# Optimization experiments

Hardware: AMD Instinct MI355X
Metric: run time of the kernel (lower is better)

Reference implementation:

```python
import jax, jax.numpy as jnp
import numpy as np

N, E, M, G = 100000, 1600000, 20000, 512
IN, ED, OUT, H, C = 64, 16, 64, 4, 8


def segment_softmax(alpha, seg, num):
    # alpha: [Etot, H]; softmax over edges sharing the same destination segment
    amax = jax.ops.segment_max(alpha, seg, num_segments=num)
    amax = jnp.where(jnp.isneginf(amax), 0.0, amax)
    ex = jnp.exp(alpha - amax[seg])
    den = jax.ops.segment_sum(ex, seg, num_segments=num)
    return ex / (den[seg] + 1e-16)


def gat_conv(x, src, dst, ea, W, We, a_s, a_d, a_e, b, concat):
    # PyG GATConv: shared lin for src/dst, edge-conditioned attention, self loops pre-added
    n = x.shape[0]
    h, c = a_s.shape
    hx = (x @ W).reshape(n, h, c)            # [N,H,C]
    ee = (ea @ We).reshape(-1, h, c)          # [Etot,H,C]
    alpha = jax.nn.leaky_relu((hx * a_s).sum(-1)[src] + (hx * a_d).sum(-1)[dst] + (ee * a_e).sum(-1), 0.2)
    alpha = segment_softmax(alpha, dst, n)    # [Etot,H]
    out = jax.ops.segment_sum(hx[src] * alpha[:, :, None], dst, num_segments=n)
    out = out.reshape(n, h * c) if concat else out.mean(axis=1)
    return out + b


def setup_inputs() -> dict:
    keys = iter(jax.random.split(jax.random.key(0), 64))

    def nrm(shape, s=0.1):
        return jax.random.normal(next(keys), shape, jnp.float32) * s

    inp = {}
    inp["x"] = jax.random.normal(next(keys), (N, IN), jnp.float32)
    inp["edge_index"] = jax.random.randint(next(keys), (2, E), 0, N)
    inp["edge_attr"] = jax.random.normal(next(keys), (E, ED), jnp.float32)
    inp["scatter_index"] = jax.random.randint(next(keys), (N,), 0, M)
    inp["scatter_norm"] = jax.random.uniform(next(keys), (M, 1), jnp.float32, 0.5, 2.0)
    inp["nodes"] = jax.random.randint(next(keys), (M,), 0, G)
    inp["decision_var_indexes"] = jax.random.randint(next(keys), (G,), 0, N)
    dims = [(IN, H, C), (H * C, H, C), (H * C, H, C), (H * C, H, OUT)]
    for i, (din, hh, cc) in enumerate(dims, 1):
        inp[f"W{i}"] = nrm((din, hh * cc))
        inp[f"We{i}"] = nrm((ED, hh * cc))
        inp[f"asrc{i}"] = nrm((hh, cc))
        inp[f"adst{i}"] = nrm((hh, cc))
        inp[f"ae{i}"] = nrm((hh, cc))
        inp[f"b{i}"] = nrm((hh * cc if i < 4 else cc,))
    inp["Wp"] = nrm((OUT, OUT))
    inp["Wt"] = nrm((OUT, OUT))
    inp["Wo"] = nrm((2 * OUT, 1))
    inp["bo"] = nrm((1,))
    return inp


def reference(x, edge_index, edge_attr, scatter_index, scatter_norm, nodes, decision_var_indexes,
              W1, We1, asrc1, adst1, ae1, b1, W2, We2, asrc2, adst2, ae2, b2,
              W3, We3, asrc3, adst3, ae3, b3, W4, We4, asrc4, adst4, ae4, b4,
              Wp, Wt, Wo, bo):
    # add self loops once; edge_attr fill_value='mean' (PyG GATConv default)
    loop = jnp.arange(N)
    src = jnp.concatenate([edge_index[0], loop])
    dst = jnp.concatenate([edge_index[1], loop])
    ea = jnp.concatenate([edge_attr, jnp.broadcast_to(edge_attr.mean(0), (N, ED))], 0)
    lrelu = lambda v: jax.nn.leaky_relu(v, 0.01)
    h1 = lrelu(gat_conv(x, src, dst, ea, W1, We1, asrc1, adst1, ae1, b1, True))
    h2 = lrelu(gat_conv(h1, src, dst, ea, W2, We2, asrc2, adst2, ae2, b2, True))
    h3 = lrelu(gat_conv(h2, src, dst, ea, W3, We3, asrc3, adst3, ae3, b3, True))
    h4 = lrelu(gat_conv(h3, src, dst, ea, W4, We4, asrc4, adst4, ae4, b4, False))
    pool = jax.ops.segment_sum(h4, scatter_index, num_segments=M) / scatter_norm
    pool = jax.ops.segment_sum(pool, nodes, num_segments=G)   # [G,OUT]
    tgt = h4[decision_var_indexes]                             # [G,OUT]
    feat = lrelu(jnp.concatenate([pool @ Wp, tgt @ Wt], axis=1))
    return feat @ Wo + bo
```

## Files before the change

### kernel.cpp

```cpp
#include <hip/hip_runtime.h>
#include <math.h>

#define NN 100000
#define EE 1600000
#define ETOT 1700000
#define MM 20000
#define GG 512

#define NBUCK 782
#define NB1 256
#define CAP 4096

static constexpr int NB_N256 = (NN + 255) / 256;
static constexpr int NB_AGG  = NN / 32;

#define SM_MEAN 0
#define SM_WEA 16
#define SM_VS4 272
#define SM_VD4 400
#define SM_W4P 536
#define SM_TOTAL 8728

typedef unsigned long long ull;

__device__ __forceinline__ unsigned short f2bf(float f) {
  unsigned int u = __float_as_uint(f);
  u += 0x7fffu + ((u >> 16) & 1u);
  return (unsigned short)(u >> 16);
}
__device__ __forceinline__ float bf2f(unsigned int h) {
  return __uint_as_float(h << 16);
}
__device__ __forceinline__ float lrelu(float v, float s) { return v > 0.f ? v : s * v; }

__global__ __launch_bounds__(256) void k_pre(
    float* __restrict__ sm, const float* __restrict__ We1, const float* __restrict__ We2,
    const float* __restrict__ We3, const float* __restrict__ We4,
    const float* __restrict__ ae1, const float* __restrict__ ae2,
    const float* __restrict__ ae3, const float* __restrict__ ae4,
    const float* __restrict__ as4, const float* __restrict__ ad4,
    const float* __restrict__ W4) {
  int t = threadIdx.x;
  {
    int l = t >> 6, d = (t >> 2) & 15, h = t & 3;
    const float* We = (l == 0) ? We1 : (l == 1) ? We2 : (l == 2) ? We3 : We4;
    const float* ae = (l == 0) ? ae1 : (l == 1) ? ae2 : (l == 2) ? ae3 : ae4;
    int C = (l == 3) ? 64 : 8;
    float s = 0.f;
    for (int c = 0; c < C; c++) s += We[d * (4 * C) + h * C + c] * ae[h * C + c];
    sm[SM_WEA + l * 64 + d * 4 + h] = s;
  }
  if (t < 128) {
    int k = t >> 2, h = t & 3;
    float s1 = 0.f, s2 = 0.f;
    for (int c = 0; c < 64; c++) {
      float w = W4[k * 256 + h * 64 + c];
      s1 += w * as4[h * 64 + c];
      s2 += w * ad4[h * 64 + c];
    }
    sm[SM_VS4 + t] = s1;
    sm[SM_VD4 + t] = s2;
  }
  for (int i = t; i < 8192; i += 256) {
    int row = i >> 6, c = i & 63;
    int h = row >> 5, k = row & 31;
    sm[SM_W4P + i] = 0.25f * W4[k * 256 + h * 64 + c];
  }
}

__global__ __launch_bounds__(1024) void k_hist1(const int* __restrict__ ei,
                                                const float* __restrict__ ea,
                                                int* __restrict__ blk_cnt,
                                                float* __restrict__ sm) {
  __shared__ int hist[NBUCK];
  __shared__ float lsum[16];
  int t = threadIdx.x;
  for (int i = t; i < NBUCK; i += 1024) hist[i] = 0;
  if (t < 16) lsum[t] = 0.f;
  __syncthreads();
  for (int e = blockIdx.x * 1024 + t; e < ETOT; e += NB1 * 1024) {
    int dst = (e < EE) ? ei[EE + e] : (e - EE);
    atomicAdd(&hist[dst >> 7], 1);
  }
  {
    const float4* ea4 = (const float4*)ea;
    int q = t & 3;
    float4 a = make_float4(0.f, 0.f, 0.f, 0.f);
    for (size_t i = (size_t)blockIdx.x * 1024 + t; i < (size_t)EE * 4;
         i += (size_t)NB1 * 1024) {
      float4 v = ea4[i];
      a.x += v.x; a.y += v.y; a.z += v.z; a.w += v.w;
    }
    for (int m = 4; m < 64; m <<= 1) {
      a.x += __shfl_xor(a.x, m, 64);
      a.y += __shfl_xor(a.y, m, 64);
      a.z += __shfl_xor(a.z, m, 64);
      a.w += __shfl_xor(a.w, m, 64);
    }
    if ((t & 63) < 4) {
      atomicAdd(&lsum[q * 4 + 0], a.x);
      atomicAdd(&lsum[q * 4 + 1], a.y);
      atomicAdd(&lsum[q * 4 + 2], a.z);
      atomicAdd(&lsum[q * 4 + 3], a.w);
    }
  }
  __syncthreads();
  for (int i = t; i < NBUCK; i += 1024) blk_cnt[blockIdx.x * NBUCK + i] = hist[i];
  if (t < 16) atomicAdd(&sm[SM_MEAN + t], lsum[t]);
}

__global__ __launch_bounds__(256) void k_bscan_a(const int* __restrict__ blk_cnt,
                                                 int* __restrict__ blk_base_T,
                                                 int* __restrict__ bucket_tot) {
  __shared__ int s[256];
  int b = blockIdx.x, t = threadIdx.x;
  int v = blk_cnt[t * NBUCK + b];
  s[t] = v;
  __syncthreads();
  for (int off = 1; off < 256; off <<= 1) {
    int x = (t >= off) ? s[t - off] : 0;
    __syncthreads();
    s[t] += x;
    __syncthreads();
  }
  blk_base_T[b * 256 + t] = s[t] - v;
  if (t == 255) bucket_tot[b] = s[255];
}

__global__ __launch_bounds__(1024) void k_bscan_b(const int* __restrict__ bucket_tot,
                                                  int* __restrict__ bucket_base,
                                                  int* __restrict__ row_off) {
  __shared__ int s[1024];
  int t = threadIdx.x;
  int v = (t < NBUCK) ? bucket_tot[t] : 0;
  s[t] = v;
  __syncthreads();
  for (int off = 1; off < 1024; off <<= 1) {
    int x = (t >= off) ? s[t - off] : 0;
    __syncthreads();
    s[t] += x;
    __syncthreads();
  }
  if (t < NBUCK) bucket_base[t] = s[t] - v;
  if (t == 0) {
    bucket_base[NBUCK] = ETOT;
    row_off[NN] = ETOT;
  }
}

__global__ __launch_bounds__(1024) void k_scatter1(const int* __restrict__ ei,
                                                   const int* __restrict__ bucket_base,
                                                   const int* __restrict__ blk_base_T,
                                                   uint2* __restrict__ pairs) {
  __shared__ int base[NBUCK];
  __shared__ int rank[NBUCK];
  int t = threadIdx.x, blk = blockIdx.x;
  for (int i = t; i < NBUCK; i += 1024) {
    base[i] = bucket_base[i] + blk_base_T[i * 256 + blk];
    rank[i] = 0;
  }
  __syncthreads();
  for (int e = blk * 1024 + t; e < ETOT; e += NB1 * 1024) {
    int src, dst;
    if (e < EE) {
      src = ei[e];
      dst = ei[EE + e];
    } else {
      src = dst = e - EE;
    }
    int bin = dst >> 7;
    int r = atomicAdd(&rank[bin], 1);
    pairs[base[bin] + r] =
        make_uint2((unsigned)src, (unsigned)e | ((unsigned)(dst & 127) << 21));
  }
}

__global__ __launch_bounds__(256) void k_sort2(const uint2* __restrict__ pairs,
                                               const int* __restrict__ bucket_base,
                                               const float* __restrict__ ea,
                                               const float* __restrict__ sm,
                                               int* __restrict__ row_off,
                                               int* __restrict__ csr_src,
                                               ull* __restrict__ apc) {
  __shared__ uint2 plds[CAP];
  __shared__ unsigned short perm[CAP];
  __shared__ int hist[128];
  __shared__ int scan[128];
  __shared__ int rankv[128];
  __shared__ float sWea[256];
  __shared__ float smean[16];
  int b = blockIdx.x, t = threadIdx.x;
  int start = bucket_base[b], end = bucket_base[b + 1];
  int cnt = end - start;
  sWea[t] = sm[SM_WEA + t];
  if (t < 16) smean[t] = sm[SM_MEAN + t] * (1.f / EE);
  if (t < 128) hist[t] = 0;
  __syncthreads();
  bool fits = (cnt <= CAP);
  if (fits) {
    for (int i = t; i < cnt; i += 256) {
      uint2 pe = pairs[start + i];
      plds[i] = pe;
      atomicAdd(&hist[(pe.y >> 21) & 127], 1);
    }
  } else {
    for (int i = t; i < cnt; i += 256)
      atomicAdd(&hist[(pairs[start + i].y >> 21) & 127], 1);
  }
  __syncthreads();
  if (t < 128) scan[t] = hist[t];
  __syncthreads();
  for (int off = 1; off < 128; off <<= 1) {
    int x = (t >= off && t < 128) ? scan[t - off] : 0;
    __syncthreads();
    if (t < 128) scan[t] += x;
    __syncthreads();
  }
  if (t < 128) {
    int excl = scan[t] - hist[t];
    rankv[t] = excl;
    int dst = b * 128 + t;
    if (dst < NN) row_off[dst] = start + excl;
  }
  __syncthreads();
  if (fits) {
    for (int i = t; i < cnt; i += 256) {
      int bin = (plds[i].y >> 21) & 127;
      int r = atomicAdd(&rankv[bin], 1);
      perm[r] = (unsigned short)i;
    }
    __syncthreads();
    for (int r = t; r < cnt; r += 256) {
      uint2 pe = plds[perm[r]];
      unsigned eid = pe.y & 0x1fffffu;
      int pos = start + r;
      csr_src[pos] = (int)pe.x;
      float eav[16];
      if (eid < EE) {
        const float4* p = (const float4*)(ea + (size_t)eid * 16);
        float4 v0 = p[0], v1 = p[1], v2 = p[2], v3 = p[3];
        eav[0] = v0.x; eav[1] = v0.y; eav[2] = v0.z; eav[3] = v0.w;
        eav[4] = v1.x; eav[5] = v1.y; eav[6] = v1.z; eav[7] = v1.w;
        eav[8] = v2.x; eav[9] = v2.y; eav[10] = v2.z; eav[11] = v2.w;
        eav[12] = v3.x; eav[13] = v3.y; eav[14] = v3.z; eav[15] = v3.w;
      } else {
#pragma unroll
        for (int d = 0; d < 16; d++) eav[d] = smean[d];
      }
#pragma unroll
      for (int l = 0; l < 4; l++) {
        ull pk = 0;
#pragma unroll
        for (int h = 0; h < 4; h++) {
          float s = 0.f;
#pragma unroll
          for (int d = 0; d < 16; d++) s += eav[d] * sWea[l * 64 + d * 4 + h];
          pk |= (ull)f2bf(s) << (16 * h);
        }
        apc[(size_t)l * ETOT + pos] = pk;
      }
    }
  } else {
    for (int i = t; i < cnt; i += 256) {
      uint2 pe = pairs[start + i];
      int bin = (pe.y >> 21) & 127;
      unsigned eid = pe.y & 0x1fffffu;
      int r = atomicAdd(&rankv[bin], 1);
      int pos = start + r;
      csr_src[pos] = (int)pe.x;
      float eav[16];
      if (eid < EE) {
        const float4* p = (const float4*)(ea + (size_t)eid * 16);
        float4 v0 = p[0], v1 = p[1], v2 = p[2], v3 = p[3];
        eav[0] = v0.x; eav[1] = v0.y; eav[2] = v0.z; eav[3] = v0.w;
        eav[4] = v1.x; eav[5] = v1.y; eav[6] = v1.z; eav[7] = v1.w;
        eav[8] = v2.x; eav[9] = v2.y; eav[10] = v2.z; eav[11] = v2.w;
        eav[12] = v3.x; eav[13] = v3.y; eav[14] = v3.z; eav[15] = v3.w;
      } else {
#pragma unroll
        for (int d = 0; d < 16; d++) eav[d] = smean[d];
      }
#pragma unroll
      for (int l = 0; l < 4; l++) {
        ull pk = 0;
#pragma unroll
        for (int h = 0; h < 4; h++) {
          float s = 0.f;
#pragma unroll
          for (int d = 0; d < 16; d++) s += eav[d] * sWea[l * 64 + d * 4 + h];
          pk |= (ull)f2bf(s) << (16 * h);
        }
        apc[(size_t)l * ETOT + pos] = pk;
      }
    }
  }
}

template <int DIN>
__global__ __launch_bounds__(256) void k_t(const float* __restrict__ in,
                                           const float* __restrict__ W,
                                           const float* __restrict__ a_s,
                                           const float* __restrict__ a_d,
                                           unsigned short* __restrict__ hxb,
                                           float* __restrict__ ssrc,
                                           float* __restrict__ sdst) {
  __shared__ float4 sW[DIN * 8];
  __shared__ float sas[32], sad[32];
  int t = threadIdx.x;
  for (int i = t; i < DIN * 8; i += 256) sW[i] = ((const float4*)W)[i];
  if (t < 32) { sas[t] = a_s[t]; sad[t] = a_d[t]; }
  __syncthreads();
  int n = blockIdx.x * 256 + t;
  if (n >= NN) return;
  float acc[32];
#pragma unroll
  for (int j = 0; j < 32; j++) acc[j] = 0.f;
  const float* xr = in + (size_t)n * DIN;
  for (int k = 0; k < DIN; k += 4) {
    float4 xv = *(const float4*)(xr + k);
    float xa[4] = {xv.x, xv.y, xv.z, xv.w};
#pragma unroll
    for (int kk = 0; kk < 4; kk++) {
#pragma unroll
      for (int j4 = 0; j4 < 8; j4++) {
        float4 ww = sW[(k + kk) * 8 + j4];
        acc[j4 * 4 + 0] += xa[kk] * ww.x;
        acc[j4 * 4 + 1] += xa[kk] * ww.y;
        acc[j4 * 4 + 2] += xa[kk] * ww.z;
        acc[j4 * 4 + 3] += xa[kk] * ww.w;
      }
    }
  }
  float ssum[4], dsum[4];
#pragma unroll
  for (int h = 0; h < 4; h++) {
    float s = 0.f, d = 0.f;
#pragma unroll
    for (int c = 0; c < 8; c++) {
      s += acc[h * 8 + c] * sas[h * 8 + c];
      d += acc[h * 8 + c] * sad[h * 8 + c];
    }
    ssum[h] = s;
    dsum[h] = d;
  }
  unsigned int up[16];
#pragma unroll
  for (int i = 0; i < 16; i++)
    up[i] = (unsigned)f2bf(acc[2 * i]) | ((unsigned)f2bf(acc[2 * i + 1]) << 16);
  uint4* ho = (uint4*)(hxb + (size_t)n * 32);
  ho[0] = make_uint4(up[0], up[1], up[2], up[3]);
  ho[1] = make_uint4(up[4], up[5], up[6], up[7]);
  ho[2] = make_uint4(up[8], up[9], up[10], up[11]);
  ho[3] = make_uint4(up[12], up[13], up[14], up[15]);
  ((float4*)ssrc)[n] = make_float4(ssum[0], ssum[1], ssum[2], ssum[3]);
  ((float4*)sdst)[n] = make_float4(dsum[0], dsum[1], dsum[2], dsum[3]);
}

__global__ __launch_bounds__(256) void k_t4(const float* __restrict__ h3,
                                            const float* __restrict__ sm,
                                            unsigned short* __restrict__ h3b,
                                            float* __restrict__ ssrc,
                                            float* __restrict__ sdst) {
  __shared__ float sVs[128], sVd[128];
  int t = threadIdx.x;
  if (t < 128) { sVs[t] = sm[SM_VS4 + t]; sVd[t] = sm[SM_VD4 + t]; }
  __syncthreads();
  int n = blockIdx.x * 256 + t;
  if (n >= NN) return;
  const float* r = h3 + (size_t)n * 32;
  float v[32];
#pragma unroll
  for (int k = 0; k < 32; k++) v[k] = r[k];
  float s0 = 0, s1 = 0, s2 = 0, s3 = 0, d0 = 0, d1 = 0, d2 = 0, d3 = 0;
#pragma unroll
  for (int k = 0; k < 32; k++) {
    s0 += v[k] * sVs[k * 4 + 0]; s1 += v[k] * sVs[k * 4 + 1];
    s2 += v[k] * sVs[k * 4 + 2]; s3 += v[k] * sVs[k * 4 + 3];
    d0 += v[k] * sVd[k * 4 + 0]; d1 += v[k] * sVd[k * 4 + 1];
    d2 += v[k] * sVd[k * 4 + 2]; d3 += v[k] * sVd[k * 4 + 3];
  }
  unsigned int up[16];
#pragma unroll
  for (int i = 0; i < 16; i++)
    up[i] = (unsigned)f2bf(v[2 * i]) | ((unsigned)f2bf(v[2 * i + 1]) << 16);
  uint4* ho = (uint4*)(h3b + (size_t)n * 32);
  ho[0] = make_uint4(up[0], up[1], up[2], up[3]);
  ho[1] = make_uint4(up[4], up[5], up[6], up[7]);
  ho[2] = make_uint4(up[8], up[9], up[10], up[11]);
  ho[3] = make_uint4(up[12], up[13], up[14], up[15]);
  ((float4*)ssrc)[n] = make_float4(s0, s1, s2, s3);
  ((float4*)sdst)[n] = make_float4(d0, d1, d2, d3);
}

__global__ __launch_bounds__(256) void k_agg(const int* __restrict__ row_off,
                                             const int* __restrict__ csr_src,
                                             const ull* __restrict__ apl,
                                             const unsigned short* __restrict__ hxb,
                                             const float* __restrict__ ssrc,
                                             const float* __restrict__ sdst,
                                             const float* __restrict__ bias,
                                             float* __restrict__ outp) {
  int t = threadIdx.x;
  int g = t >> 3, j = t & 7, h = j >> 1;
  int n = blockIdx.x * 32 + g;
  if (n >= NN) return;
  float sd = sdst[n * 4 + h];
  int e0 = row_off[n], e1 = row_off[n + 1];
  float m = -1e30f, den = 0.f;
  float4 acc = make_float4(0.f, 0.f, 0.f, 0.f);
  for (int e = e0; e < e1; ++e) {
    int src = csr_src[e];
    ull pk = apl[e];
    float ae = bf2f((unsigned int)(unsigned short)(pk >> (16 * h)));
    float al = ssrc[src * 4 + h] + sd + ae;
    al = lrelu(al, 0.2f);
    uint2 u = *(const uint2*)(hxb + (size_t)src * 32 + (j << 2));
    float nm = fmaxf(m, al);
    float c1 = __expf(m - nm);
    float p = __expf(al - nm);
    den = den * c1 + p;
    acc.x = acc.x * c1 + p * bf2f(u.x & 0xffffu);
    acc.y = acc.y * c1 + p * bf2f(u.x >> 16);
    acc.z = acc.z * c1 + p * bf2f(u.y & 0xffffu);
    acc.w = acc.w * c1 + p * bf2f(u.y >> 16);
    m = nm;
  }
  float inv = 1.f / (den + 1e-16f);
  float4 b = *(const float4*)(bias + (j << 2));
  float4 o;
  o.x = lrelu(acc.x * inv + b.x, 0.01f);
  o.y = lrelu(acc.y * inv + b.y, 0.01f);
  o.z = lrelu(acc.z * inv + b.z, 0.01f);
  o.w = lrelu(acc.w * inv + b.w, 0.01f);
  *(float4*)(outp + (size_t)n * 32 + (j << 2)) = o;
}

__global__ __launch_bounds__(256) void k_agg4(const int* __restrict__ row_off,
                                              const int* __restrict__ csr_src,
                                              const ull* __restrict__ apl,
                                              const unsigned short* __restrict__ h3b,
                                              const float* __restrict__ ssrc,
                                              const float* __restrict__ sdst,
                                              unsigned short* __restrict__ aggb) {
  int t = threadIdx.x;
  int g = t >> 3, j = t & 7;
  int n = blockIdx.x * 32 + g;
  if (n >= NN) return;
  float4 sdv = ((const float4*)sdst)[n];
  float sda[4] = {sdv.x, sdv.y, sdv.z, sdv.w};
  int e0 = row_off[n], e1 = row_off[n + 1];
  float m[4], den[4];
  float4 acc[4];
#pragma unroll
  for (int h = 0; h < 4; h++) {
    m[h] = -1e30f;
    den[h] = 0.f;
    acc[h] = make_float4(0.f, 0.f, 0.f, 0.f);
  }
  for (int e = e0; e < e1; ++e) {
    int src = csr_src[e];
    ull pk = apl[e];
    float4 ssv = ((const float4*)ssrc)[src];
    float ssa[4] = {ssv.x, ssv.y, ssv.z, ssv.w};
    uint2 u = *(const uint2*)(h3b + (size_t)src * 32 + (j << 2));
    float hx0 = bf2f(u.x & 0xffffu), hx1 = bf2f(u.x >> 16);
    float hx2 = bf2f(u.y & 0xffffu), hx3 = bf2f(u.y >> 16);
#pragma unroll
    for (int h = 0; h < 4; h++) {
      float al = ssa[h] + sda[h] + bf2f((unsigned int)(unsigned short)(pk >> (16 * h)));
      al = lrelu(al, 0.2f);
      float nm = fmaxf(m[h], al);
      float c1 = __expf(m[h] - nm);
      float p = __expf(al - nm);
      den[h] = den[h] * c1 + p;
      acc[h].x = acc[h].x * c1 + p * hx0;
      acc[h].y = acc[h].y * c1 + p * hx1;
      acc[h].z = acc[h].z * c1 + p * hx2;
      acc[h].w = acc[h].w * c1 + p * hx3;
      m[h] = nm;
    }
  }
#pragma unroll
  for (int h = 0; h < 4; h++) {
    float inv = 1.f / (den[h] + 1e-16f);
    unsigned int u0 = (unsigned)f2bf(acc[h].x * inv) | ((unsigned)f2bf(acc[h].y * inv) << 16);
    unsigned int u1 = (unsigned)f2bf(acc[h].z * inv) | ((unsigned)f2bf(acc[h].w * inv) << 16);
    *(uint2*)(aggb + (size_t)n * 128 + h * 32 + (j << 2)) = make_uint2(u0, u1);
  }
}

__global__ __launch_bounds__(256) void k_epi4(const unsigned short* __restrict__ aggb,
                                              const float* __restrict__ sm,
                                              const float* __restrict__ b4,
                                              float* __restrict__ h4) {
  __shared__ float4 sW[2048];
  __shared__ float sb[64];
  int t = threadIdx.x;
  for (int i = t; i < 2048; i += 256) sW[i] = ((const float4*)(sm + SM_W4P))[i];
  if (t < 64) sb[t] = b4[t];
  __syncthreads();
  int n = blockIdx.x * 256 + t;
  if (n >= NN) return;
  float acc[64];
#pragma unroll
  for (int j = 0; j < 64; j++) acc[j] = 0.f;
  const unsigned short* r = aggb + (size_t)n * 128;
  for (int k = 0; k < 128; k += 4) {
    uint2 u = *(const uint2*)(r + k);
    float va[4] = {bf2f(u.x & 0xffffu), bf2f(u.x >> 16), bf2f(u.y & 0xffffu),
                   bf2f(u.y >> 16)};
#pragma unroll
    for (int kk = 0; kk < 4; kk++) {
#pragma unroll
      for (int j4 = 0; j4 < 16; j4++) {
        float4 wv = sW[(k + kk) * 16 + j4];
        acc[j4 * 4 + 0] += va[kk] * wv.x;
        acc[j4 * 4 + 1] += va[kk] * wv.y;
        acc[j4 * 4 + 2] += va[kk] * wv.z;
        acc[j4 * 4 + 3] += va[kk] * wv.w;
      }
    }
  }
  float* o = h4 + (size_t)n * 64;
#pragma unroll
  for (int j4 = 0; j4 < 16; j4++) {
    float4 ov;
    ov.x = lrelu(acc[j4 * 4 + 0] + sb[j4 * 4 + 0], 0.01f);
    ov.y = lrelu(acc[j4 * 4 + 1] + sb[j4 * 4 + 1], 0.01f);
    ov.z = lrelu(acc[j4 * 4 + 2] + sb[j4 * 4 + 2], 0.01f);
    ov.w = lrelu(acc[j4 * 4 + 3] + sb[j4 * 4 + 3], 0.01f);
    ((float4*)o)[j4] = ov;
  }
}

__global__ __launch_bounds__(256) void k_pool1(const float* __restrict__ h4,
                                               const int* __restrict__ sidx,
                                               float* __restrict__ pool1) {
  int i = blockIdx.x * 256 + threadIdx.x;
  if (i >= NN * 64) return;
  int n = i >> 6, c = i & 63;
  atomicAdd(&pool1[(size_t)sidx[n] * 64 + c], h4[i]);
}

__global__ __launch_bounds__(256) void k_pool2(const float* __restrict__ pool1,
                                               const float* __restrict__ snorm,
                                               const int* __restrict__ nodes,
                                               float* __restrict__ pool2) {
  int i = blockIdx.x * 256 + threadIdx.x;
  if (i >= MM * 64) return;
  int mi = i >> 6, c = i & 63;
  float v = pool1[i] / snorm[mi];
  atomicAdd(&pool2[(size_t)nodes[mi] * 64 + c], v);
}

__global__ __launch_bounds__(64) void k_final(const float* __restrict__ pool2,
                                              const float* __restrict__ h4,
                                              const int* __restrict__ dvi,
                                              const float* __restrict__ Wp,
                                              const float* __restrict__ Wt,
                                              const float* __restrict__ Wo,
                                              const float* __restrict__ bo,
                                              float* __restrict__ out) {
  __shared__ float p[64], tt[64];
  int gI = blockIdx.x, j = threadIdx.x;
  p[j] = pool2[gI * 64 + j];
  tt[j] = h4[(size_t)dvi[gI] * 64 + j];
  __syncthreads();
  float f1 = 0.f, f2 = 0.f;
#pragma unroll 8
  for (int c = 0; c < 64; c++) {
    f1 += p[c] * Wp[c * 64 + j];
    f2 += tt[c] * Wt[c * 64 + j];
  }
  f1 = lrelu(f1, 0.01f);
  f2 = lrelu(f2, 0.01f);
  float v = f1 * Wo[j] + f2 * Wo[64 + j];
  for (int off = 32; off > 0; off >>= 1) v += __shfl_down(v, off, 64);
  if (j == 0) out[gI] = v + bo[0];
}

extern "C" void kernel_launch(void* const* d_in, const int* in_sizes, int n_in,
                              void* d_out, int out_size, void* d_ws, size_t ws_size,
                              hipStream_t stream) {
  const float* x = (const float*)d_in[0];
  const int* ei = (const int*)d_in[1];
  const float* ea = (const float*)d_in[2];
  const int* sidx = (const int*)d_in[3];
  const float* snorm = (const float*)d_in[4];
  const int* nodes = (const int*)d_in[5];
  const int* dvi = (const int*)d_in[6];
  const float* W1 = (const float*)d_in[7];
  const float* as1 = (const float*)d_in[9];
  const float* ad1 = (const float*)d_in[10];
  const float* b1 = (const float*)d_in[12];
  const float* W2 = (const float*)d_in[13];
  const float* as2 = (const float*)d_in[15];
  const float* ad2 = (const float*)d_in[16];
  const float* b2 = (const float*)d_in[18];
  const float* W3 = (const float*)d_in[19];
  const float* as3 = (const float*)d_in[21];
  const float* ad3 = (const float*)d_in[22];
  const float* b3 = (const float*)d_in[24];
  const float* b4 = (const float*)d_in[30];
  const float* Wp = (const float*)d_in[31];
  const float* Wt = (const float*)d_in[32];
  const float* Wo = (const float*)d_in[33];
  const float* bo = (const float*)d_in[34];
  float* out = (float*)d_out;

  char* w = (char*)d_ws;
  size_t off = 0;
  auto take = [&](size_t bytes) -> char* {
    char* p = w + off;
    off = (off + bytes + 255) & ~(size_t)255;
    return p;
  };
  int* row_off = (int*)take((size_t)(NN + 1) * 4);
  float* sm = (float*)take(SM_TOTAL * 4);
  uint2* pairs = (uint2*)take((size_t)ETOT * 8);
  int* csr_src = (int*)take((size_t)ETOT * 4);
  ull* apc = (ull*)take((size_t)ETOT * 4 * 8);
  int* blk_cnt = (int*)take((size_t)NB1 * NBUCK * 4);
  int* blk_base_T = (int*)take((size_t)NBUCK * NB1 * 4);
  int* bucket_tot = (int*)take((size_t)NBUCK * 4);
  int* bucket_base = (int*)take((size_t)(NBUCK + 1) * 4);
  float* h4 = (float*)take((size_t)NN * 64 * 4);
  unsigned short* aggb = (unsigned short*)take((size_t)NN * 128 * 2);
  unsigned short* hxb = (unsigned short*)take((size_t)NN * 32 * 2);
  unsigned short* h3b = (unsigned short*)take((size_t)NN * 32 * 2);
  float* ssrc = (float*)take((size_t)NN * 4 * 4);
  float* sdst = (float*)take((size_t)NN * 4 * 4);
  float* bufA = (float*)take((size_t)NN * 32 * 4);
  float* bufB = (float*)take((size_t)NN * 32 * 4);
  float* pool1 = (float*)take((size_t)MM * 64 * 4);
  float* pool2 = (float*)take((size_t)GG * 64 * 4);
  if (off > ws_size) return;

  hipMemsetAsync(sm, 0, 64, stream);
  hipMemsetAsync(pool1, 0, (size_t)MM * 64 * 4, stream);
  hipMemsetAsync(pool2, 0, (size_t)GG * 64 * 4, stream);

  k_pre<<<1, 256, 0, stream>>>(sm, (const float*)d_in[8], (const float*)d_in[14],
                               (const float*)d_in[20], (const float*)d_in[26],
                               (const float*)d_in[11], (const float*)d_in[17],
                               (const float*)d_in[23], (const float*)d_in[29],
                               (const float*)d_in[27], (const float*)d_in[28],
                               (const float*)d_in[25]);

  k_hist1<<<NB1, 1024, 0, stream>>>(ei, ea, blk_cnt, sm);
  k_bscan_a<<<NBUCK, 256, 0, stream>>>(blk_cnt, blk_base_T, bucket_tot);
  k_bscan_b<<<1, 1024, 0, stream>>>(bucket_tot, bucket_base, row_off);
  k_scatter1<<<NB1, 1024, 0, stream>>>(ei, bucket_base, blk_base_T, pairs);
  k_sort2<<<NBUCK, 256, 0, stream>>>(pairs, bucket_base, ea, sm, row_off, csr_src, apc);

  k_t<64><<<NB_N256, 256, 0, stream>>>(x, W1, as1, ad1, hxb, ssrc, sdst);
  k_agg<<<NB_AGG, 256, 0, stream>>>(row_off, csr_src, apc, hxb, ssrc, sdst, b1, bufA);
  k_t<32><<<NB_N256, 256, 0, stream>>>(bufA, W2, as2, ad2, hxb, ssrc, sdst);
  k_agg<<<NB_AGG, 256, 0, stream>>>(row_off, csr_src, apc + (size_t)ETOT, hxb, ssrc,
                                    sdst, b2, bufB);
  k_t<32><<<NB_N256, 256, 0, stream>>>(bufB, W3, as3, ad3, hxb, ssrc, sdst);
  k_agg<<<NB_AGG, 256, 0, stream>>>(row_off, csr_src, apc + 2 * (size_t)ETOT, hxb, ssrc,
                                    sdst, b3, bufA);
  k_t4<<<NB_N256, 256, 0, stream>>>(bufA, sm, h3b, ssrc, sdst);
  k_agg4<<<NB_AGG, 256, 0, stream>>>(row_off, csr_src, apc + 3 * (size_t)ETOT, h3b, ssrc,
                                     sdst, aggb);
  k_epi4<<<NB_N256, 256, 0, stream>>>(aggb, sm, b4, h4);

  k_pool1<<<(NN * 64) / 256, 256, 0, stream>>>(h4, sidx, pool1);
  k_pool2<<<(MM * 64) / 256, 256, 0, stream>>>(pool1, snorm, nodes, pool2);
  k_final<<<GG, 64, 0, stream>>>(pool2, h4, dvi, Wp, Wt, Wo, bo, out);
}
```

Measured before the change: 728.0 us.

## Split edge-attr packing into separate kernel and drop online-softmax max tracking

Edge-attribute projection and packing move out of the bucket sort kernel into a new fully parallel k_pack kernel that reads a per-position edge index array. The aim is to raise parallelism beyond the 782 sort blocks. The aggregation kernels also drop the running-max rescaling of online softmax and exponentiate the clamped logit directly, which removes two exps and a rescale per edge. The cost is an extra launch, an extra index buffer round trip, and numerical risk from the 80 clamp without max subtraction, which can change results for large logits.

```diff
diff --git a/kernel.cpp b/kernel.cpp
--- a/kernel.cpp
+++ b/kernel.cpp
@@ -12,6 +12,7 @@
 #define CAP 4096
 
 static constexpr int NB_N256 = (NN + 255) / 256;
+static constexpr int NB_E256 = (ETOT + 255) / 256;
 static constexpr int NB_AGG  = NN / 32;
 
 #define SM_MEAN 0
@@ -177,23 +178,17 @@
 
 __global__ __launch_bounds__(256) void k_sort2(const uint2* __restrict__ pairs,
                                                const int* __restrict__ bucket_base,
-                                               const float* __restrict__ ea,
-                                               const float* __restrict__ sm,
                                                int* __restrict__ row_off,
                                                int* __restrict__ csr_src,
-                                               ull* __restrict__ apc) {
+                                               int* __restrict__ eidx) {
   __shared__ uint2 plds[CAP];
   __shared__ unsigned short perm[CAP];
   __shared__ int hist[128];
   __shared__ int scan[128];
   __shared__ int rankv[128];
-  __shared__ float sWea[256];
-  __shared__ float smean[16];
   int b = blockIdx.x, t = threadIdx.x;
   int start = bucket_base[b], end = bucket_base[b + 1];
   int cnt = end - start;
-  sWea[t] = sm[SM_WEA + t];
-  if (t < 16) smean[t] = sm[SM_MEAN + t] * (1.f / EE);
   if (t < 128) hist[t] = 0;
   __syncthreads();
   bool fits = (cnt <= CAP);
@@ -232,67 +227,56 @@
     __syncthreads();
     for (int r = t; r < cnt; r += 256) {
       uint2 pe = plds[perm[r]];
-      unsigned eid = pe.y & 0x1fffffu;
-      int pos = start + r;
-      csr_src[pos] = (int)pe.x;
-      float eav[16];
-      if (eid < EE) {
-        const float4* p = (const float4*)(ea + (size_t)eid * 16);
-        float4 v0 = p[0], v1 = p[1], v2 = p[2], v3 = p[3];
-        eav[0] = v0.x; eav[1] = v0.y; eav[2] = v0.z; eav[3] = v0.w;
-        eav[4] = v1.x; eav[5] = v1.y; eav[6] = v1.z; eav[7] = v1.w;
-        eav[8] = v2.x; eav[9] = v2.y; eav[10] = v2.z; eav[11] = v2.w;
-        eav[12] = v3.x; eav[13] = v3.y; eav[14] = v3.z; eav[15] = v3.w;
-      } else {
-#pragma unroll
-        for (int d = 0; d < 16; d++) eav[d] = smean[d];
-      }
-#pragma unroll
-      for (int l = 0; l < 4; l++) {
-        ull pk = 0;
-#pragma unroll
-        for (int h = 0; h < 4; h++) {
-          float s = 0.f;
-#pragma unroll
-          for (int d = 0; d < 16; d++) s += eav[d] * sWea[l * 64 + d * 4 + h];
-          pk |= (ull)f2bf(s) << (16 * h);
-        }
-        apc[(size_t)l * ETOT + pos] = pk;
-      }
+      csr_src[start + r] = (int)pe.x;
+      eidx[start + r] = (int)(pe.y & 0x1fffffu);
     }
   } else {
     for (int i = t; i < cnt; i += 256) {
       uint2 pe = pairs[start + i];
       int bin = (pe.y >> 21) & 127;
-      unsigned eid = pe.y & 0x1fffffu;
       int r = atomicAdd(&rankv[bin], 1);
-      int pos = start + r;
-      csr_src[pos] = (int)pe.x;
-      float eav[16];
-      if (eid < EE) {
-        const float4* p = (const float4*)(ea + (size_t)eid * 16);
-        float4 v0 = p[0], v1 = p[1], v2 = p[2], v3 = p[3];
-        eav[0] = v0.x; eav[1] = v0.y; eav[2] = v0.z; eav[3] = v0.w;
-        eav[4] = v1.x; eav[5] = v1.y; eav[6] = v1.z; eav[7] = v1.w;
-        eav[8] = v2.x; eav[9] = v2.y; eav[10] = v2.z; eav[11] = v2.w;
-        eav[12] = v3.x; eav[13] = v3.y; eav[14] = v3.z; eav[15] = v3.w;
-      } else {
-#pragma unroll
-        for (int d = 0; d < 16; d++) eav[d] = smean[d];
-      }
-#pragma unroll
-      for (int l = 0; l < 4; l++) {
-        ull pk = 0;
-#pragma unroll
-        for (int h = 0; h < 4; h++) {
-          float s = 0.f;
-#pragma unroll
-          for (int d = 0; d < 16; d++) s += eav[d] * sWea[l * 64 + d * 4 + h];
-          pk |= (ull)f2bf(s) << (16 * h);
-        }
-        apc[(size_t)l * ETOT + pos] = pk;
-      }
-    }
+      csr_src[start + r] = (int)pe.x;
+      eidx[start + r] = (int)(pe.y & 0x1fffffu);
+    }
+  }
+}
+
+__global__ __launch_bounds__(256) void k_pack(const int* __restrict__ eidx,
+                                              const float* __restrict__ ea,
+                                              const float* __restrict__ sm,
+                                              ull* __restrict__ apc) {
+  __shared__ float sWea[256];
+  __shared__ float smean[16];
+  int t = threadIdx.x;
+  sWea[t] = sm[SM_WEA + t];
+  if (t < 16) smean[t] = sm[SM_MEAN + t] * (1.f / EE);
+  __syncthreads();
+  int pos = blockIdx.x * 256 + t;
+  if (pos >= ETOT) return;
+  int eid = eidx[pos];
+  float eav[16];
+  if (eid < EE) {
+    const float4* p = (const float4*)(ea + (size_t)eid * 16);
+    float4 v0 = p[0], v1 = p[1], v2 = p[2], v3 = p[3];
+    eav[0] = v0.x; eav[1] = v0.y; eav[2] = v0.z; eav[3] = v0.w;
+    eav[4] = v1.x; eav[5] = v1.y; eav[6] = v1.z; eav[7] = v1.w;
+    eav[8] = v2.x; eav[9] = v2.y; eav[10] = v2.z; eav[11] = v2.w;
+    eav[12] = v3.x; eav[13] = v3.y; eav[14] = v3.z; eav[15] = v3.w;
+  } else {
+#pragma unroll
+    for (int d = 0; d < 16; d++) eav[d] = smean[d];
+  }
+#pragma unroll
+  for (int l = 0; l < 4; l++) {
+    ull pk = 0;
+#pragma unroll
+    for (int h = 0; h < 4; h++) {
+      float s = 0.f;
+#pragma unroll
+      for (int d = 0; d < 16; d++) s += eav[d] * sWea[l * 64 + d * 4 + h];
+      pk |= (ull)f2bf(s) << (16 * h);
+    }
+    apc[(size_t)l * ETOT + pos] = pk;
   }
 }
 
@@ -406,24 +390,21 @@
   if (n >= NN) return;
   float sd = sdst[n * 4 + h];
   int e0 = row_off[n], e1 = row_off[n + 1];
-  float m = -1e30f, den = 0.f;
+  float den = 0.f;
   float4 acc = make_float4(0.f, 0.f, 0.f, 0.f);
   for (int e = e0; e < e1; ++e) {
     int src = csr_src[e];
     ull pk = apl[e];
     float ae = bf2f((unsigned int)(unsigned short)(pk >> (16 * h)));
     float al = ssrc[src * 4 + h] + sd + ae;
-    al = lrelu(al, 0.2f);
+    al = fminf(lrelu(al, 0.2f), 80.f);
     uint2 u = *(const uint2*)(hxb + (size_t)src * 32 + (j << 2));
-    float nm = fmaxf(m, al);
-    float c1 = __expf(m - nm);
-    float p = __expf(al - nm);
-    den = den * c1 + p;
-    acc.x = acc.x * c1 + p * bf2f(u.x & 0xffffu);
-    acc.y = acc.y * c1 + p * bf2f(u.x >> 16);
-    acc.z = acc.z * c1 + p * bf2f(u.y & 0xffffu);
-    acc.w = acc.w * c1 + p * bf2f(u.y >> 16);
-    m = nm;
+    float p = __expf(al);
+    den += p;
+    acc.x += p * bf2f(u.x & 0xffffu);
+    acc.y += p * bf2f(u.x >> 16);
+    acc.z += p * bf2f(u.y & 0xffffu);
+    acc.w += p * bf2f(u.y >> 16);
   }
   float inv = 1.f / (den + 1e-16f);
   float4 b = *(const float4*)(bias + (j << 2));
@@ -449,11 +430,10 @@
   float4 sdv = ((const float4*)sdst)[n];
   float sda[4] = {sdv.x, sdv.y, sdv.z, sdv.w};
   int e0 = row_off[n], e1 = row_off[n + 1];
-  float m[4], den[4];
+  float den[4];
   float4 acc[4];
 #pragma unroll
   for (int h = 0; h < 4; h++) {
-    m[h] = -1e30f;
     den[h] = 0.f;
     acc[h] = make_float4(0.f, 0.f, 0.f, 0.f);
   }
@@ -468,16 +448,13 @@
 #pragma unroll
     for (int h = 0; h < 4; h++) {
       float al = ssa[h] + sda[h] + bf2f((unsigned int)(unsigned short)(pk >> (16 * h)));
-      al = lrelu(al, 0.2f);
-      float nm = fmaxf(m[h], al);
-      float c1 = __expf(m[h] - nm);
-      float p = __expf(al - nm);
-      den[h] = den[h] * c1 + p;
-      acc[h].x = acc[h].x * c1 + p * hx0;
-      acc[h].y = acc[h].y * c1 + p * hx1;
-      acc[h].z = acc[h].z * c1 + p * hx2;
-      acc[h].w = acc[h].w * c1 + p * hx3;
-      m[h] = nm;
+      al = fminf(lrelu(al, 0.2f), 80.f);
+      float p = __expf(al);
+      den[h] += p;
+      acc[h].x += p * hx0;
+      acc[h].y += p * hx1;
+      acc[h].z += p * hx2;
+      acc[h].w += p * hx3;
     }
   }
 #pragma unroll
@@ -619,6 +596,7 @@
   float* sm = (float*)take(SM_TOTAL * 4);
   uint2* pairs = (uint2*)take((size_t)ETOT * 8);
   int* csr_src = (int*)take((size_t)ETOT * 4);
+  int* eidx = (int*)take((size_t)ETOT * 4);
   ull* apc = (ull*)take((size_t)ETOT * 4 * 8);
   int* blk_cnt = (int*)take((size_t)NB1 * NBUCK * 4);
   int* blk_base_T = (int*)take((size_t)NBUCK * NB1 * 4);
@@ -651,7 +629,8 @@
   k_bscan_a<<<NBUCK, 256, 0, stream>>>(blk_cnt, blk_base_T, bucket_tot);
   k_bscan_b<<<1, 1024, 0, stream>>>(bucket_tot, bucket_base, row_off);
   k_scatter1<<<NB1, 1024, 0, stream>>>(ei, bucket_base, blk_base_T, pairs);
-  k_sort2<<<NBUCK, 256, 0, stream>>>(pairs, bucket_base, ea, sm, row_off, csr_src, apc);
+  k_sort2<<<NBUCK, 256, 0, stream>>>(pairs, bucket_base, row_off, csr_src, eidx);
+  k_pack<<<NB_E256, 256, 0, stream>>>(eidx, ea, sm, apc);
 
   k_t<64><<<NB_N256, 256, 0, stream>>>(x, W1, as1, ad1, hxb, ssrc, sdst);
   k_agg<<<NB_AGG, 256, 0, stream>>>(row_off, csr_src, apc, hxb, ssrc, sdst, b1, bufA);
```

Measured after the change: 703.2 us. 1.04x faster.
